# Performance work log

Hardware: AMD Instinct MI355X
Metric: run time of the kernel (lower is better)

## Reference

```python
import jax, jax.numpy as jnp
import numpy as np

B = 16384       # batch
G = 8           # groups
S = 16          # state_c (per-group in/out channels)
H = 512         # hidden_c (per-group hidden channels)
FACTOR = 1.0
SWISH_DIV = 1.1


def setup_inputs() -> dict:
    key = jax.random.key(0)
    ks = jax.random.split(key, 12)
    def w(k, shape, fan_in):
        bound = 1.0 / np.sqrt(fan_in)
        return jax.random.uniform(k, shape, jnp.float32, -bound, bound)
    return {
        "x":  jax.random.normal(ks[0], (B, G * S), dtype=jnp.float32),
        # grouped 1x1 convs as per-group linear weights [G, out_c, in_c]
        "W1": w(ks[1], (G, H, S), S), "b1": w(ks[2], (G, H), S),
        "beta1": jnp.full((G,), 0.5, jnp.float32),
        "W2": w(ks[3], (G, H, H), H), "b2": w(ks[4], (G, H), H),
        "beta2": jnp.full((G,), 0.5, jnp.float32),
        "W3": w(ks[5], (G, H, H), H), "b3": w(ks[6], (G, H), H),
        "beta3": jnp.full((G,), 0.5, jnp.float32),
        "W4": w(ks[7], (G, S, H), H), "b4": w(ks[8], (G, S), H),
    }


def _group_swish(x, beta):
    # x: [B, G, C]; beta: [G] -> y = x * sigmoid(x * softplus(beta)) / 1.1
    sp = jax.nn.softplus(beta)[None, :, None]
    return x * jax.nn.sigmoid(x * sp) / SWISH_DIV


def reference(x, W1, b1, beta1, W2, b2, beta2, W3, b3, beta3, W4, b4):
    h = x.reshape(-1, G, S)                                   # [B,G,S]
    h = jnp.einsum('bgs,ghs->bgh', h, W1) + b1[None]          # [B,G,H]
    h = _group_swish(h, beta1)
    h = jnp.einsum('bgi,goi->bgo', h, W2) + b2[None]
    h = _group_swish(h, beta2)
    h = jnp.einsum('bgi,goi->bgo', h, W3) + b3[None]
    h = _group_swish(h, beta3)
    h = jnp.einsum('bgh,gsh->bgs', h, W4) + b4[None]          # [B,G,S]
    return h.reshape(-1, G * S) * FACTOR
```

## Files before the change

kernel.cpp:

```cpp
#include <hip/hip_runtime.h>
#include <stdint.h>

#define G_ 8
#define S_ 16
#define H_ 512
#define TB 64
#define NTH 512

typedef _Float16 h16;
typedef _Float16 h16x8 __attribute__((ext_vector_type(8)));
typedef float f32x4 __attribute__((ext_vector_type(4)));
typedef float f32x16 __attribute__((ext_vector_type(16)));

#define XB_STRIDE 24
#define HB_BYTES (TB * 1024)
#define SMEM_BYTES (HB_BYTES + TB * XB_STRIDE * 2)

__device__ __forceinline__ float swishf(float v, float sp) {
    const float e = __expf(-v * sp);
    return v * __builtin_amdgcn_rcpf(1.0f + e) * (1.0f / 1.1f);
}

__device__ __forceinline__ uint32_t pk16(float a, float b) {
    return __builtin_bit_cast(uint32_t, __builtin_amdgcn_cvt_pkrtz(a, b));
}

__device__ __forceinline__ uint32_t hswz(int row, uint32_t byte_in_row) {
    return (uint32_t)row * 1024u + (byte_in_row ^ (((uint32_t)(row & 7)) << 4));
}

template<bool USEWS>
__device__ __forceinline__ h16x8 loadA32(const h16* __restrict__ wpk,
                                         const float* __restrict__ wf,
                                         int nb, int ks, int ln, int KB, int Ksrc) {
    if constexpr (USEWS) {
        return *(const h16x8*)(wpk + (((size_t)nb * KB + ks) * 64 + ln) * 8);
    } else {
        const int row = nb * 32 + (ln & 31);
        const int k = ks * 16 + (ln >> 5) * 8;
        const float* p = wf + (size_t)row * Ksrc + k;
        h16x8 r;
        #pragma unroll
        for (int j = 0; j < 8; ++j) r[j] = (h16)p[j];
        return r;
    }
}

template<bool USEWS>
__device__ __forceinline__ h16x8 loadA16(const h16* __restrict__ wpk,
                                         const float* __restrict__ wf,
                                         int ks32, int ln, int Ksrc) {
    if constexpr (USEWS) {
        return *(const h16x8*)(wpk + ((size_t)ks32 * 64 + ln) * 8);
    } else {
        const int row = ln & 15;
        const int k = ks32 * 32 + (ln >> 4) * 8;
        const float* p = wf + (size_t)row * Ksrc + k;
        h16x8 r;
        #pragma unroll
        for (int j = 0; j < 8; ++j) r[j] = (h16)p[j];
        return r;
    }
}

__device__ __forceinline__ void swish_store32(const f32x16 (&acc)[2][2], char* hb,
                                              const float* __restrict__ bias, float sp,
                                              int wc0, int ln) {
    const int l31 = ln & 31, lh = ln >> 5;
    #pragma unroll
    for (int ot = 0; ot < 2; ++ot) {
        #pragma unroll
        for (int rq = 0; rq < 4; ++rq) {
            const int col0 = wc0 + ot * 32 + rq * 8 + lh * 4;
            const f32x4 bv = *(const f32x4*)(bias + col0);
            #pragma unroll
            for (int bt = 0; bt < 2; ++bt) {
                const int b = bt * 32 + l31;
                const float v0 = swishf(acc[ot][bt][rq * 4 + 0] + bv[0], sp);
                const float v1 = swishf(acc[ot][bt][rq * 4 + 1] + bv[1], sp);
                const float v2 = swishf(acc[ot][bt][rq * 4 + 2] + bv[2], sp);
                const float v3 = swishf(acc[ot][bt][rq * 4 + 3] + bv[3], sp);
                const uint64_t u = (uint64_t)pk16(v0, v1)
                                 | ((uint64_t)pk16(v2, v3) << 32);
                *(uint64_t*)(hb + hswz(b, (uint32_t)(col0 * 2))) = u;
            }
        }
    }
}

template<bool USEWS>
__device__ __forceinline__ void layerH32(f32x16 (&acc)[2][2],
                                         const h16* __restrict__ wpk, const float* __restrict__ wf,
                                         const char* __restrict__ hb, int wc0, int ln) {
    const int l31 = ln & 31, lh = ln >> 5;
    const int cB = wc0 >> 5;
    #pragma unroll
    for (int ot = 0; ot < 2; ++ot)
        #pragma unroll
        for (int bt = 0; bt < 2; ++bt) acc[ot][bt] = (f32x16)(0.f);

    #pragma unroll 4
    for (int ks = 0; ks < 32; ++ks) {
        const h16x8 a0 = loadA32<USEWS>(wpk, wf, cB + 0, ks, ln, 32, H_);
        const h16x8 a1 = loadA32<USEWS>(wpk, wf, cB + 1, ks, ln, 32, H_);
        const h16x8 b0 = *(const h16x8*)(hb + hswz(l31,      (uint32_t)(ks * 32 + lh * 16)));
        const h16x8 b1 = *(const h16x8*)(hb + hswz(32 + l31, (uint32_t)(ks * 32 + lh * 16)));
        __builtin_amdgcn_s_setprio(1);
        acc[0][0] = __builtin_amdgcn_mfma_f32_32x32x16_f16(a0, b0, acc[0][0], 0, 0, 0);
        acc[0][1] = __builtin_amdgcn_mfma_f32_32x32x16_f16(a0, b1, acc[0][1], 0, 0, 0);
        acc[1][0] = __builtin_amdgcn_mfma_f32_32x32x16_f16(a1, b0, acc[1][0], 0, 0, 0);
        acc[1][1] = __builtin_amdgcn_mfma_f32_32x32x16_f16(a1, b1, acc[1][1], 0, 0, 0);
        __builtin_amdgcn_s_setprio(0);
    }
}

template<bool USEWS>
__global__ __launch_bounds__(NTH, 4) void mlp_fused(
    const float* __restrict__ x,
    const float* __restrict__ W1f, const float* __restrict__ b1, const float* __restrict__ be1,
    const float* __restrict__ W2f, const float* __restrict__ b2, const float* __restrict__ be2,
    const float* __restrict__ W3f, const float* __restrict__ b3, const float* __restrict__ be3,
    const float* __restrict__ W4f, const float* __restrict__ b4,
    const h16* __restrict__ W1p, const h16* __restrict__ W2p,
    const h16* __restrict__ W3p, const h16* __restrict__ W4p,
    float* __restrict__ out) {
    extern __shared__ char smem[];
    h16* __restrict__ xb = (h16*)(smem + HB_BYTES);

    const int bid = blockIdx.x;
    const int g = bid & 7;
    const int rowbase = (bid >> 3) * TB;
    const int tid = threadIdx.x;
    const int wv = tid >> 6;
    const int ln = tid & 63;
    const int l31 = ln & 31;
    const int lh = ln >> 5;
    const int wc0 = wv * 64;

    const float sp1 = log1pf(__expf(be1[g]));
    const float sp2 = log1pf(__expf(be2[g]));
    const float sp3 = log1pf(__expf(be3[g]));

    const h16* w1p = W1p + (size_t)g * H_ * S_;
    const h16* w2p = W2p + (size_t)g * H_ * H_;
    const h16* w3p = W3p + (size_t)g * H_ * H_;
    const h16* w4p = W4p + (size_t)g * S_ * H_;
    const float* w1f = W1f + (size_t)g * H_ * S_;
    const float* w2f = W2f + (size_t)g * H_ * H_;
    const float* w3f = W3f + (size_t)g * H_ * H_;
    const float* w4f = W4f + (size_t)g * S_ * H_;

    {
        const int idx = tid * 2;
        const int r = idx >> 4, s = idx & 15;
        const float2 v = *(const float2*)(x + (size_t)(rowbase + r) * (G_ * S_) + g * S_ + s);
        *(uint32_t*)((char*)xb + (r * XB_STRIDE + s) * 2) = pk16(v.x, v.y);
    }
    __syncthreads();

    f32x16 acc[2][2];

    {
        #pragma unroll
        for (int ot = 0; ot < 2; ++ot)
            #pragma unroll
            for (int bt = 0; bt < 2; ++bt) acc[ot][bt] = (f32x16)(0.f);
        h16x8 aW[2], bX[2];
        #pragma unroll
        for (int ot = 0; ot < 2; ++ot)
            aW[ot] = loadA32<USEWS>(w1p, w1f, (wc0 >> 5) + ot, 0, ln, 1, S_);
        #pragma unroll
        for (int bt = 0; bt < 2; ++bt)
            bX[bt] = *(const h16x8*)(xb + (bt * 32 + l31) * XB_STRIDE + lh * 8);
        #pragma unroll
        for (int ot = 0; ot < 2; ++ot)
            #pragma unroll
            for (int bt = 0; bt < 2; ++bt)
                acc[ot][bt] = __builtin_amdgcn_mfma_f32_32x32x16_f16(aW[ot], bX[bt],
                                                                     acc[ot][bt], 0, 0, 0);
    }
    swish_store32(acc, smem, b1 + g * H_, sp1, wc0, ln);
    __syncthreads();

    layerH32<USEWS>(acc, w2p, w2f, smem, wc0, ln);
    __syncthreads();
    swish_store32(acc, smem, b2 + g * H_, sp2, wc0, ln);
    __syncthreads();

    layerH32<USEWS>(acc, w3p, w3f, smem, wc0, ln);
    __syncthreads();
    swish_store32(acc, smem, b3 + g * H_, sp3, wc0, ln);
    __syncthreads();

    if (wv < 4) {
        f32x4 a4 = {0.f, 0.f, 0.f, 0.f};
        const int l15 = ln & 15, lq = ln >> 4;
        #pragma unroll 4
        for (int ks = 0; ks < 16; ++ks) {
            const h16x8 a = loadA16<USEWS>(w4p, w4f, ks, ln, H_);
            const h16x8 b = *(const h16x8*)(smem + hswz(wv * 16 + l15,
                                                        (uint32_t)(ks * 64 + lq * 16)));
            a4 = __builtin_amdgcn_mfma_f32_16x16x32_f16(a, b, a4, 0, 0, 0);
        }
        const int brow = wv * 16 + l15;
        const int s0 = lq * 4;
        const f32x4 bv = *(const f32x4*)(b4 + g * S_ + s0);
        f32x4 o4;
        #pragma unroll
        for (int r = 0; r < 4; ++r) o4[r] = a4[r] + bv[r];
        *(f32x4*)(out + (size_t)(rowbase + brow) * (G_ * S_) + g * S_ + s0) = o4;
    }
}

__global__ void packW32(const float* __restrict__ s, h16* __restrict__ d,
                        int NB_total, int KB, int Ks) {
    const int t = blockIdx.x * 256 + threadIdx.x;
    const int total = NB_total * KB * 64;
    if (t >= total) return;
    const int ln = t & 63;
    const int blk = t >> 6;
    const int kb = blk % KB;
    const int nbg = blk / KB;
    const int row = nbg * 32 + (ln & 31);
    const int k = kb * 16 + (ln >> 5) * 8;
    const float* p = s + (size_t)row * Ks + k;
    h16x8 o;
    #pragma unroll
    for (int j = 0; j < 8; ++j) o[j] = (h16)p[j];
    *(h16x8*)(d + (size_t)t * 8) = o;
}

__global__ void packW16(const float* __restrict__ s, h16* __restrict__ d,
                        int NB_total, int KB, int Ks) {
    const int t = blockIdx.x * 256 + threadIdx.x;
    const int total = NB_total * KB * 64;
    if (t >= total) return;
    const int ln = t & 63;
    const int blk = t >> 6;
    const int kb = blk % KB;
    const int nbg = blk / KB;
    const int row = nbg * 16 + (ln & 15);
    const int k = kb * 32 + (ln >> 4) * 8;
    const float* p = s + (size_t)row * Ks + k;
    h16x8 o;
    #pragma unroll
    for (int j = 0; j < 8; ++j) o[j] = (h16)p[j];
    *(h16x8*)(d + (size_t)t * 8) = o;
}

extern "C" void kernel_launch(void* const* d_in, const int* in_sizes, int n_in,
                              void* d_out, int out_size, void* d_ws, size_t ws_size,
                              hipStream_t stream) {
    const float* x   = (const float*)d_in[0];
    const float* W1  = (const float*)d_in[1];
    const float* b1  = (const float*)d_in[2];
    const float* be1 = (const float*)d_in[3];
    const float* W2  = (const float*)d_in[4];
    const float* b2  = (const float*)d_in[5];
    const float* be2 = (const float*)d_in[6];
    const float* W3  = (const float*)d_in[7];
    const float* b3  = (const float*)d_in[8];
    const float* be3 = (const float*)d_in[9];
    const float* W4  = (const float*)d_in[10];
    const float* b4  = (const float*)d_in[11];
    float* out = (float*)d_out;

    const size_t nW2  = (size_t)G_ * H_ * H_;
    const size_t nW1p = (size_t)G_ * H_ * S_;
    const size_t nW4  = (size_t)G_ * S_ * H_;
    const size_t need = (2 * nW2 + nW1p + nW4) * sizeof(h16);

    const dim3 grid(2048), blk(NTH);

    if (ws_size >= need) {
        h16* W2p = (h16*)d_ws;
        h16* W3p = W2p + nW2;
        h16* W1p = W3p + nW2;
        h16* W4p = W1p + nW1p;
        packW32<<<dim3((unsigned)((nW2 / 8 + 255) / 256)), dim3(256), 0, stream>>>(W2, W2p, G_ * 16, 32, H_);
        packW32<<<dim3((unsigned)((nW2 / 8 + 255) / 256)), dim3(256), 0, stream>>>(W3, W3p, G_ * 16, 32, H_);
        packW32<<<dim3((unsigned)((nW1p / 8 + 255) / 256)), dim3(256), 0, stream>>>(W1, W1p, G_ * 16, 1, S_);
        packW16<<<dim3((unsigned)((nW4 / 8 + 255) / 256)), dim3(256), 0, stream>>>(W4, W4p, G_, 16, H_);
        (void)hipFuncSetAttribute(reinterpret_cast<const void*>(mlp_fused<true>),
                                  hipFuncAttributeMaxDynamicSharedMemorySize, (int)SMEM_BYTES);
        mlp_fused<true><<<grid, blk, SMEM_BYTES, stream>>>(
            x, W1, b1, be1, W2, b2, be2, W3, b3, be3, W4, b4,
            W1p, W2p, W3p, W4p, out);
    } else {
        (void)hipFuncSetAttribute(reinterpret_cast<const void*>(mlp_fused<false>),
                                  hipFuncAttributeMaxDynamicSharedMemorySize, (int)SMEM_BYTES);
        mlp_fused<false><<<grid, blk, SMEM_BYTES, stream>>>(
            x, W1, b1, be1, W2, b2, be2, W3, b3, be3, W4, b4,
            nullptr, nullptr, nullptr, nullptr, out);
    }
}
```

Before: 200.0 us.

## Retile hidden layers to four output tiles per wave and repack weights ks-major

Each wave now computes 128 output columns for 32 batch rows, instead of 64 columns for all 64 rows. Per K-step it issues four weight fragment loads and one LDS activation load, where before it issued two of each. The packed weight layout is reordered ks-major so a wave's four consecutive weight fragments are contiguous in memory. This trades fewer LDS reads per MFMA for each weight tile now being fetched by two waves per block, which doubles global/L2 weight traffic.

```diff
diff --git a/kernel.cpp b/kernel.cpp
--- a/kernel.cpp
+++ b/kernel.cpp
@@ -30,11 +30,11 @@
 }
 
 template<bool USEWS>
-__device__ __forceinline__ h16x8 loadA32(const h16* __restrict__ wpk,
-                                         const float* __restrict__ wf,
-                                         int nb, int ks, int ln, int KB, int Ksrc) {
+__device__ __forceinline__ h16x8 loadA32ks(const h16* __restrict__ wpk,
+                                           const float* __restrict__ wf,
+                                           int ks, int nb, int ln, int Ksrc) {
     if constexpr (USEWS) {
-        return *(const h16x8*)(wpk + (((size_t)nb * KB + ks) * 64 + ln) * 8);
+        return *(const h16x8*)(wpk + (((size_t)ks * 16 + nb) * 64 + ln) * 8);
     } else {
         const int row = nb * 32 + (ln & 31);
         const int k = ks * 16 + (ln >> 5) * 8;
@@ -63,53 +63,49 @@
     }
 }
 
-__device__ __forceinline__ void swish_store32(const f32x16 (&acc)[2][2], char* hb,
+__device__ __forceinline__ void swish_store32(const f32x16 (&acc)[4], char* hb,
                                               const float* __restrict__ bias, float sp,
-                                              int wc0, int ln) {
+                                              int os, int bh, int ln) {
     const int l31 = ln & 31, lh = ln >> 5;
-    #pragma unroll
-    for (int ot = 0; ot < 2; ++ot) {
+    const int b = bh * 32 + l31;
+    #pragma unroll
+    for (int nb = 0; nb < 4; ++nb) {
         #pragma unroll
         for (int rq = 0; rq < 4; ++rq) {
-            const int col0 = wc0 + ot * 32 + rq * 8 + lh * 4;
+            const int col0 = os * 128 + nb * 32 + rq * 8 + lh * 4;
             const f32x4 bv = *(const f32x4*)(bias + col0);
-            #pragma unroll
-            for (int bt = 0; bt < 2; ++bt) {
-                const int b = bt * 32 + l31;
-                const float v0 = swishf(acc[ot][bt][rq * 4 + 0] + bv[0], sp);
-                const float v1 = swishf(acc[ot][bt][rq * 4 + 1] + bv[1], sp);
-                const float v2 = swishf(acc[ot][bt][rq * 4 + 2] + bv[2], sp);
-                const float v3 = swishf(acc[ot][bt][rq * 4 + 3] + bv[3], sp);
-                const uint64_t u = (uint64_t)pk16(v0, v1)
-                                 | ((uint64_t)pk16(v2, v3) << 32);
-                *(uint64_t*)(hb + hswz(b, (uint32_t)(col0 * 2))) = u;
-            }
+            const float v0 = swishf(acc[nb][rq * 4 + 0] + bv[0], sp);
+            const float v1 = swishf(acc[nb][rq * 4 + 1] + bv[1], sp);
+            const float v2 = swishf(acc[nb][rq * 4 + 2] + bv[2], sp);
+            const float v3 = swishf(acc[nb][rq * 4 + 3] + bv[3], sp);
+            const uint64_t u = (uint64_t)pk16(v0, v1)
+                             | ((uint64_t)pk16(v2, v3) << 32);
+            *(uint64_t*)(hb + hswz(b, (uint32_t)(col0 * 2))) = u;
         }
     }
 }
 
 template<bool USEWS>
-__device__ __forceinline__ void layerH32(f32x16 (&acc)[2][2],
+__device__ __forceinline__ void layerH32(f32x16 (&acc)[4],
                                          const h16* __restrict__ wpk, const float* __restrict__ wf,
-                                         const char* __restrict__ hb, int wc0, int ln) {
+                                         const char* __restrict__ hb, int os, int bh, int ln) {
     const int l31 = ln & 31, lh = ln >> 5;
-    const int cB = wc0 >> 5;
-    #pragma unroll
-    for (int ot = 0; ot < 2; ++ot)
-        #pragma unroll
-        for (int bt = 0; bt < 2; ++bt) acc[ot][bt] = (f32x16)(0.f);
+    const int brow = bh * 32 + l31;
+    #pragma unroll
+    for (int nb = 0; nb < 4; ++nb) acc[nb] = (f32x16)(0.f);
 
     #pragma unroll 4
     for (int ks = 0; ks < 32; ++ks) {
-        const h16x8 a0 = loadA32<USEWS>(wpk, wf, cB + 0, ks, ln, 32, H_);
-        const h16x8 a1 = loadA32<USEWS>(wpk, wf, cB + 1, ks, ln, 32, H_);
-        const h16x8 b0 = *(const h16x8*)(hb + hswz(l31,      (uint32_t)(ks * 32 + lh * 16)));
-        const h16x8 b1 = *(const h16x8*)(hb + hswz(32 + l31, (uint32_t)(ks * 32 + lh * 16)));
+        h16x8 a0 = loadA32ks<USEWS>(wpk, wf, ks, os * 4 + 0, ln, H_);
+        h16x8 a1 = loadA32ks<USEWS>(wpk, wf, ks, os * 4 + 1, ln, H_);
+        h16x8 a2 = loadA32ks<USEWS>(wpk, wf, ks, os * 4 + 2, ln, H_);
+        h16x8 a3 = loadA32ks<USEWS>(wpk, wf, ks, os * 4 + 3, ln, H_);
+        const h16x8 b = *(const h16x8*)(hb + hswz(brow, (uint32_t)(ks * 32 + lh * 16)));
         __builtin_amdgcn_s_setprio(1);
-        acc[0][0] = __builtin_amdgcn_mfma_f32_32x32x16_f16(a0, b0, acc[0][0], 0, 0, 0);
-        acc[0][1] = __builtin_amdgcn_mfma_f32_32x32x16_f16(a0, b1, acc[0][1], 0, 0, 0);
-        acc[1][0] = __builtin_amdgcn_mfma_f32_32x32x16_f16(a1, b0, acc[1][0], 0, 0, 0);
-        acc[1][1] = __builtin_amdgcn_mfma_f32_32x32x16_f16(a1, b1, acc[1][1], 0, 0, 0);
+        acc[0] = __builtin_amdgcn_mfma_f32_32x32x16_f16(a0, b, acc[0], 0, 0, 0);
+        acc[1] = __builtin_amdgcn_mfma_f32_32x32x16_f16(a1, b, acc[1], 0, 0, 0);
+        acc[2] = __builtin_amdgcn_mfma_f32_32x32x16_f16(a2, b, acc[2], 0, 0, 0);
+        acc[3] = __builtin_amdgcn_mfma_f32_32x32x16_f16(a3, b, acc[3], 0, 0, 0);
         __builtin_amdgcn_s_setprio(0);
     }
 }
@@ -135,7 +131,8 @@
     const int ln = tid & 63;
     const int l31 = ln & 31;
     const int lh = ln >> 5;
-    const int wc0 = wv * 64;
+    const int os = wv & 3;
+    const int bh = wv >> 2;
 
     const float sp1 = log1pf(__expf(be1[g]));
     const float sp2 = log1pf(__expf(be2[g]));
@@ -158,38 +155,31 @@
     }
     __syncthreads();
 
-    f32x16 acc[2][2];
+    f32x16 acc[4];
 
     {
         #pragma unroll
-        for (int ot = 0; ot < 2; ++ot)
-            #pragma unroll
-            for (int bt = 0; bt < 2; ++bt) acc[ot][bt] = (f32x16)(0.f);
-        h16x8 aW[2], bX[2];
-        #pragma unroll
-        for (int ot = 0; ot < 2; ++ot)
-            aW[ot] = loadA32<USEWS>(w1p, w1f, (wc0 >> 5) + ot, 0, ln, 1, S_);
-        #pragma unroll
-        for (int bt = 0; bt < 2; ++bt)
-            bX[bt] = *(const h16x8*)(xb + (bt * 32 + l31) * XB_STRIDE + lh * 8);
-        #pragma unroll
-        for (int ot = 0; ot < 2; ++ot)
-            #pragma unroll
-            for (int bt = 0; bt < 2; ++bt)
-                acc[ot][bt] = __builtin_amdgcn_mfma_f32_32x32x16_f16(aW[ot], bX[bt],
-                                                                     acc[ot][bt], 0, 0, 0);
-    }
-    swish_store32(acc, smem, b1 + g * H_, sp1, wc0, ln);
-    __syncthreads();
-
-    layerH32<USEWS>(acc, w2p, w2f, smem, wc0, ln);
-    __syncthreads();
-    swish_store32(acc, smem, b2 + g * H_, sp2, wc0, ln);
-    __syncthreads();
-
-    layerH32<USEWS>(acc, w3p, w3f, smem, wc0, ln);
-    __syncthreads();
-    swish_store32(acc, smem, b3 + g * H_, sp3, wc0, ln);
+        for (int nb = 0; nb < 4; ++nb) acc[nb] = (f32x16)(0.f);
+        h16x8 aW[4];
+        #pragma unroll
+        for (int nb = 0; nb < 4; ++nb)
+            aW[nb] = loadA32ks<USEWS>(w1p, w1f, 0, os * 4 + nb, ln, S_);
+        const h16x8 bX = *(const h16x8*)(xb + (bh * 32 + l31) * XB_STRIDE + lh * 8);
+        #pragma unroll
+        for (int nb = 0; nb < 4; ++nb)
+            acc[nb] = __builtin_amdgcn_mfma_f32_32x32x16_f16(aW[nb], bX, acc[nb], 0, 0, 0);
+    }
+    swish_store32(acc, smem, b1 + g * H_, sp1, os, bh, ln);
+    __syncthreads();
+
+    layerH32<USEWS>(acc, w2p, w2f, smem, os, bh, ln);
+    __syncthreads();
+    swish_store32(acc, smem, b2 + g * H_, sp2, os, bh, ln);
+    __syncthreads();
+
+    layerH32<USEWS>(acc, w3p, w3f, smem, os, bh, ln);
+    __syncthreads();
+    swish_store32(acc, smem, b3 + g * H_, sp3, os, bh, ln);
     __syncthreads();
 
     if (wv < 4) {
@@ -213,16 +203,18 @@
 }
 
 __global__ void packW32(const float* __restrict__ s, h16* __restrict__ d,
-                        int NB_total, int KB, int Ks) {
+                        int KB, int Ks) {
     const int t = blockIdx.x * 256 + threadIdx.x;
-    const int total = NB_total * KB * 64;
+    const int total = G_ * KB * 16 * 64;
     if (t >= total) return;
     const int ln = t & 63;
     const int blk = t >> 6;
-    const int kb = blk % KB;
-    const int nbg = blk / KB;
-    const int row = nbg * 32 + (ln & 31);
-    const int k = kb * 16 + (ln >> 5) * 8;
+    const int nb = blk & 15;
+    const int rest = blk >> 4;
+    const int ks = rest % KB;
+    const int g = rest / KB;
+    const int row = g * H_ + nb * 32 + (ln & 31);
+    const int k = ks * 16 + (ln >> 5) * 8;
     const float* p = s + (size_t)row * Ks + k;
     h16x8 o;
     #pragma unroll
@@ -277,9 +269,9 @@
         h16* W3p = W2p + nW2;
         h16* W1p = W3p + nW2;
         h16* W4p = W1p + nW1p;
-        packW32<<<dim3((unsigned)((nW2 / 8 + 255) / 256)), dim3(256), 0, stream>>>(W2, W2p, G_ * 16, 32, H_);
-        packW32<<<dim3((unsigned)((nW2 / 8 + 255) / 256)), dim3(256), 0, stream>>>(W3, W3p, G_ * 16, 32, H_);
-        packW32<<<dim3((unsigned)((nW1p / 8 + 255) / 256)), dim3(256), 0, stream>>>(W1, W1p, G_ * 16, 1, S_);
+        packW32<<<dim3((unsigned)((nW2 / 8 + 255) / 256)), dim3(256), 0, stream>>>(W2, W2p, 32, H_);
+        packW32<<<dim3((unsigned)((nW2 / 8 + 255) / 256)), dim3(256), 0, stream>>>(W3, W3p, 32, H_);
+        packW32<<<dim3((unsigned)((nW1p / 8 + 255) / 256)), dim3(256), 0, stream>>>(W1, W1p, 1, S_);
         packW16<<<dim3((unsigned)((nW4 / 8 + 255) / 256)), dim3(256), 0, stream>>>(W4, W4p, G_, 16, H_);
         (void)hipFuncSetAttribute(reinterpret_cast<const void*>(mlp_fused<true>),
                                   hipFuncAttributeMaxDynamicSharedMemorySize, (int)SMEM_BYTES);
```

Result: slower. 237.9 us (+18.9%).

## Prefetch weight fragments one k-step ahead, reorder packed weights, widen LDS swizzle

Applied to the files above, without the earlier changes.

The hidden-layer GEMM loop now loads the next k-step's weight fragments into registers while the current MFMAs run, so global-load latency is overlapped with compute. The packed weight layout becomes k-step-major within each group, so the 16 column blocks for one k-step sit next to each other in memory. The LDS XOR swizzle now uses row&31 instead of row&7, spreading the B-fragment reads over more banks. In exchange the loop holds extra live registers and issues one redundant prefetch on its final iteration.

```diff
diff --git a/kernel.cpp b/kernel.cpp
--- a/kernel.cpp
+++ b/kernel.cpp
@@ -26,15 +26,15 @@
 }
 
 __device__ __forceinline__ uint32_t hswz(int row, uint32_t byte_in_row) {
-    return (uint32_t)row * 1024u + (byte_in_row ^ (((uint32_t)(row & 7)) << 4));
+    return (uint32_t)row * 1024u + (byte_in_row ^ (((uint32_t)(row & 31)) << 4));
 }
 
 template<bool USEWS>
-__device__ __forceinline__ h16x8 loadA32(const h16* __restrict__ wpk,
-                                         const float* __restrict__ wf,
-                                         int nb, int ks, int ln, int KB, int Ksrc) {
+__device__ __forceinline__ h16x8 loadA32ks(const h16* __restrict__ wpk,
+                                           const float* __restrict__ wf,
+                                           int ks, int nb, int ln, int Ksrc) {
     if constexpr (USEWS) {
-        return *(const h16x8*)(wpk + (((size_t)nb * KB + ks) * 64 + ln) * 8);
+        return *(const h16x8*)(wpk + (((size_t)ks * 16 + nb) * 64 + ln) * 8);
     } else {
         const int row = nb * 32 + (ln & 31);
         const int k = ks * 16 + (ln >> 5) * 8;
@@ -91,26 +91,31 @@
 template<bool USEWS>
 __device__ __forceinline__ void layerH32(f32x16 (&acc)[2][2],
                                          const h16* __restrict__ wpk, const float* __restrict__ wf,
-                                         const char* __restrict__ hb, int wc0, int ln) {
+                                         const char* __restrict__ hb, int os, int ln) {
     const int l31 = ln & 31, lh = ln >> 5;
-    const int cB = wc0 >> 5;
+    const int nb0 = os * 2;
     #pragma unroll
     for (int ot = 0; ot < 2; ++ot)
         #pragma unroll
         for (int bt = 0; bt < 2; ++bt) acc[ot][bt] = (f32x16)(0.f);
 
-    #pragma unroll 4
+    h16x8 aC0 = loadA32ks<USEWS>(wpk, wf, 0, nb0 + 0, ln, H_);
+    h16x8 aC1 = loadA32ks<USEWS>(wpk, wf, 0, nb0 + 1, ln, H_);
+
+    #pragma unroll 2
     for (int ks = 0; ks < 32; ++ks) {
-        const h16x8 a0 = loadA32<USEWS>(wpk, wf, cB + 0, ks, ln, 32, H_);
-        const h16x8 a1 = loadA32<USEWS>(wpk, wf, cB + 1, ks, ln, 32, H_);
+        const int ksn = (ks + 1 < 32) ? ks + 1 : 0;
+        h16x8 aN0 = loadA32ks<USEWS>(wpk, wf, ksn, nb0 + 0, ln, H_);
+        h16x8 aN1 = loadA32ks<USEWS>(wpk, wf, ksn, nb0 + 1, ln, H_);
         const h16x8 b0 = *(const h16x8*)(hb + hswz(l31,      (uint32_t)(ks * 32 + lh * 16)));
         const h16x8 b1 = *(const h16x8*)(hb + hswz(32 + l31, (uint32_t)(ks * 32 + lh * 16)));
         __builtin_amdgcn_s_setprio(1);
-        acc[0][0] = __builtin_amdgcn_mfma_f32_32x32x16_f16(a0, b0, acc[0][0], 0, 0, 0);
-        acc[0][1] = __builtin_amdgcn_mfma_f32_32x32x16_f16(a0, b1, acc[0][1], 0, 0, 0);
-        acc[1][0] = __builtin_amdgcn_mfma_f32_32x32x16_f16(a1, b0, acc[1][0], 0, 0, 0);
-        acc[1][1] = __builtin_amdgcn_mfma_f32_32x32x16_f16(a1, b1, acc[1][1], 0, 0, 0);
+        acc[0][0] = __builtin_amdgcn_mfma_f32_32x32x16_f16(aC0, b0, acc[0][0], 0, 0, 0);
+        acc[0][1] = __builtin_amdgcn_mfma_f32_32x32x16_f16(aC0, b1, acc[0][1], 0, 0, 0);
+        acc[1][0] = __builtin_amdgcn_mfma_f32_32x32x16_f16(aC1, b0, acc[1][0], 0, 0, 0);
+        acc[1][1] = __builtin_amdgcn_mfma_f32_32x32x16_f16(aC1, b1, acc[1][1], 0, 0, 0);
         __builtin_amdgcn_s_setprio(0);
+        aC0 = aN0; aC1 = aN1;
     }
 }
 
@@ -168,7 +173,7 @@
         h16x8 aW[2], bX[2];
         #pragma unroll
         for (int ot = 0; ot < 2; ++ot)
-            aW[ot] = loadA32<USEWS>(w1p, w1f, (wc0 >> 5) + ot, 0, ln, 1, S_);
+            aW[ot] = loadA32ks<USEWS>(w1p, w1f, 0, wv * 2 + ot, ln, S_);
         #pragma unroll
         for (int bt = 0; bt < 2; ++bt)
             bX[bt] = *(const h16x8*)(xb + (bt * 32 + l31) * XB_STRIDE + lh * 8);
@@ -182,12 +187,12 @@
     swish_store32(acc, smem, b1 + g * H_, sp1, wc0, ln);
     __syncthreads();
 
-    layerH32<USEWS>(acc, w2p, w2f, smem, wc0, ln);
+    layerH32<USEWS>(acc, w2p, w2f, smem, wv, ln);
     __syncthreads();
     swish_store32(acc, smem, b2 + g * H_, sp2, wc0, ln);
     __syncthreads();
 
-    layerH32<USEWS>(acc, w3p, w3f, smem, wc0, ln);
+    layerH32<USEWS>(acc, w3p, w3f, smem, wv, ln);
     __syncthreads();
     swish_store32(acc, smem, b3 + g * H_, sp3, wc0, ln);
     __syncthreads();
@@ -213,16 +218,18 @@
 }
 
 __global__ void packW32(const float* __restrict__ s, h16* __restrict__ d,
-                        int NB_total, int KB, int Ks) {
+                        int KB, int Ks) {
     const int t = blockIdx.x * 256 + threadIdx.x;
-    const int total = NB_total * KB * 64;
+    const int total = G_ * KB * 16 * 64;
     if (t >= total) return;
     const int ln = t & 63;
     const int blk = t >> 6;
-    const int kb = blk % KB;
-    const int nbg = blk / KB;
-    const int row = nbg * 32 + (ln & 31);
-    const int k = kb * 16 + (ln >> 5) * 8;
+    const int nb = blk & 15;
+    const int rest = blk >> 4;
+    const int ks = rest % KB;
+    const int g = rest / KB;
+    const int row = g * H_ + nb * 32 + (ln & 31);
+    const int k = ks * 16 + (ln >> 5) * 8;
     const float* p = s + (size_t)row * Ks + k;
     h16x8 o;
     #pragma unroll
@@ -277,9 +284,9 @@
         h16* W3p = W2p + nW2;
         h16* W1p = W3p + nW2;
         h16* W4p = W1p + nW1p;
-        packW32<<<dim3((unsigned)((nW2 / 8 + 255) / 256)), dim3(256), 0, stream>>>(W2, W2p, G_ * 16, 32, H_);
-        packW32<<<dim3((unsigned)((nW2 / 8 + 255) / 256)), dim3(256), 0, stream>>>(W3, W3p, G_ * 16, 32, H_);
-        packW32<<<dim3((unsigned)((nW1p / 8 + 255) / 256)), dim3(256), 0, stream>>>(W1, W1p, G_ * 16, 1, S_);
+        packW32<<<dim3((unsigned)((nW2 / 8 + 255) / 256)), dim3(256), 0, stream>>>(W2, W2p, 32, H_);
+        packW32<<<dim3((unsigned)((nW2 / 8 + 255) / 256)), dim3(256), 0, stream>>>(W3, W3p, 32, H_);
+        packW32<<<dim3((unsigned)((nW1p / 8 + 255) / 256)), dim3(256), 0, stream>>>(W1, W1p, 1, S_);
         packW16<<<dim3((unsigned)((nW4 / 8 + 255) / 256)), dim3(256), 0, stream>>>(W4, W4p, G_, 16, H_);
         (void)hipFuncSetAttribute(reinterpret_cast<const void*>(mlp_fused<true>),
                                   hipFuncAttributeMaxDynamicSharedMemorySize, (int)SMEM_BYTES);
```

After: 197.2 us. Within noise of the previous version (-1.4%).
